# Kernel optimization log

Measured on AMD Instinct MI355X. Metric: run time of the kernel, lower is better.

## Reference

```python
import jax, jax.numpy as jnp
import numpy as np

B, H, S, DK = 2, 16, 2048, 64

def setup_inputs() -> dict:
    key = jax.random.key(0)
    kq, kk, kv, km = jax.random.split(key, 4)
    queries = jax.random.normal(kq, (B, H, S, DK), dtype=jnp.float32)
    keys = jax.random.normal(kk, (B, H, S, DK), dtype=jnp.float32)
    values = jax.random.normal(kv, (B, H, S, DK), dtype=jnp.float32)
    mask = jax.random.randint(km, (B, S, S), 0, 2, dtype=jnp.int32)
    return {"queries": queries, "keys": keys, "values": values, "mask": mask}

def reference(queries, keys, values, mask):
    d_k = queries.shape[-1]
    scale = 1.0 / np.sqrt(d_k).astype(np.float32)
    # [B,H,S,S]
    scores = jnp.einsum('bhqd,bhkd->bhqk', queries, keys) * scale
    m = mask[:, None, :, :]  # broadcast over heads, like mask.unsqueeze(1)
    scores = jnp.where(m == 0, jnp.asarray(-1e9, scores.dtype), scores)
    attn = jax.nn.softmax(scores, axis=-1)
    return jnp.einsum('bhqk,bhkd->bhqd', attn, values)
```

## Files before the change

### kernel.cpp

```cpp
#include <hip/hip_runtime.h>


#define S_   2048
#define D_   64
#define H_   16
#define B_   2
#define BH_  32
#define KVB  64
#define NKV  (S_/KVB)
#define QPB  128
#define NQT  (S_/QPB)

#define KSCALE 0.18033688f

typedef __attribute__((ext_vector_type(8)))  _Float16 f16x8;
typedef __attribute__((ext_vector_type(4)))  _Float16 f16x4;
typedef __attribute__((ext_vector_type(2)))  _Float16 f16x2;
typedef __attribute__((ext_vector_type(4)))  float    f32x4;
typedef __attribute__((ext_vector_type(16))) float    f32x16;
typedef __attribute__((ext_vector_type(4)))  unsigned u32x4;

static __device__ __forceinline__ void async16(const void* g, void* l) {
  __builtin_amdgcn_global_load_lds(
      (const __attribute__((address_space(1))) void*)g,
      (__attribute__((address_space(3))) void*)l, 16, 0, 0);
}

static __device__ __forceinline__ f16x2 pkrtz(float a, float b) {
  return __builtin_bit_cast(f16x2, __builtin_amdgcn_cvt_pkrtz(a, b));
}

static __device__ __forceinline__ void plswap(unsigned& a, unsigned& b, int h) {
#if __has_builtin(__builtin_amdgcn_permlane32_swap)
  auto r = __builtin_amdgcn_permlane32_swap(a, b, false, false);
  a = (unsigned)r[0];
  b = (unsigned)r[1];
#else
  unsigned sa = __shfl_xor(a, 32), sb = __shfl_xor(b, 32);
  unsigned na = h ? sb : a, nb = h ? b : sa;
  a = na; b = nb;
#endif
}

__global__ __launch_bounds__(256) void prepass_k(
    const float* __restrict__ K, const float* __restrict__ V,
    const int* __restrict__ M,
    _Float16* __restrict__ Kh, _Float16* __restrict__ Vth,
    unsigned long long* __restrict__ Mb) {
  __shared__ float tile[64][65];
  const int bidx = blockIdx.x;
  const int tid = threadIdx.x;
  if (bidx < 1024) {
    int st = bidx & 31;
    int bh = bidx >> 5;
    const float* src = V + ((size_t)bh * S_ + st * 64) * D_;
    int r = tid >> 2, cq = tid & 3;
#pragma unroll
    for (int j = 0; j < 4; ++j) {
      float4 v = ((const float4*)(src + (size_t)r * D_))[cq + 4 * j];
      int col = (cq + 4 * j) * 4;
      tile[r][col + 0] = v.x; tile[r][col + 1] = v.y;
      tile[r][col + 2] = v.z; tile[r][col + 3] = v.w;
    }
    __syncthreads();
    int d = tid >> 2, s = (tid & 3) * 16;
    _Float16 tmp[16];
#pragma unroll
    for (int j = 0; j < 16; ++j) tmp[j] = (_Float16)tile[s + j][d];
    _Float16* dstp = Vth + ((size_t)bh * D_ + d) * S_ + st * 64 + s;
    *(f16x8*)(dstp)     = *((f16x8*)tmp);
    *(f16x8*)(dstp + 8) = *((f16x8*)tmp + 1);
  } else if (bidx < 1536) {
    int idx = (bidx - 1024) * 256 + tid;
#pragma unroll
    for (int j = 0; j < 8; ++j) {
      int i = idx + j * 131072;
      float4 v = ((const float4*)K)[i];
      f16x4 o = {(_Float16)(v.x * KSCALE), (_Float16)(v.y * KSCALE),
                 (_Float16)(v.z * KSCALE), (_Float16)(v.w * KSCALE)};
      *(f16x4*)(Kh + 4 * (size_t)i) = o;
    }
  } else {
    int lane = tid & 63;
    int wb = (bidx - 1536) * 256 + (tid >> 6) * 64;
    for (int i = 0; i < 64; ++i) {
      int w = wb + i;
      int m = M[(size_t)w * 64 + lane];
      unsigned long long bal = __ballot(m != 0);
      if (lane == 0) Mb[w] = bal;
    }
  }
}

__global__ __launch_bounds__(256, 2) void attn_fwd(
    const float* __restrict__ Qf, const _Float16* __restrict__ Kh,
    const _Float16* __restrict__ Vth, const unsigned long long* __restrict__ Mb,
    float* __restrict__ Out) {
  __shared__ _Float16 Ks[3][KVB * D_];
  __shared__ _Float16 Vs[3][D_ * KVB];
  __shared__ unsigned long long MLUT[16];

  const int tid = threadIdx.x;
  const int lane = tid & 63;
  const int h = lane >> 5;
  const int c5 = lane & 31;
  const int c7 = c5 & 7;

  if (tid < 16) {
    unsigned w0 = ((tid & 1) ? 0x3C00u : 0u) | ((tid & 2) ? 0x3C000000u : 0u);
    unsigned w1 = ((tid & 4) ? 0x3C00u : 0u) | ((tid & 8) ? 0x3C000000u : 0u);
    MLUT[tid] = (unsigned long long)w0 | ((unsigned long long)w1 << 32);
  }

  int bid = blockIdx.x;
  bid = (bid & 7) * 64 + (bid >> 3);
  const int qt = bid & (NQT - 1);
  const int bh = bid >> 4;
  const int b = bh >> 4;

  const int q = qt * QPB + (tid >> 6) * 32 + c5;

  f16x8 qf[4];
  {
    const float* qp = Qf + ((size_t)bh * S_ + q) * D_ + 8 * h;
#pragma unroll
    for (int dc = 0; dc < 4; ++dc) {
      _Float16 t[8];
#pragma unroll
      for (int j = 0; j < 8; ++j) t[j] = (_Float16)qp[16 * dc + j];
      qf[dc] = *(f16x8*)t;
    }
  }

  f32x16 accO0, accO1;
#pragma unroll
  for (int e = 0; e < 16; ++e) { accO0[e] = 0.f; accO1[e] = 0.f; }
  float l_run = 0.f;

  const int srow = tid >> 3, sgr = tid & 7;
  const int gs = (sgr ^ (srow & 7)) << 3;
  const _Float16* kp = Kh + (size_t)bh * S_ * D_ + (size_t)srow * D_ + gs;
  const _Float16* vp = Vth + (size_t)bh * D_ * S_ + (size_t)srow * S_ + gs;
  const int ldso = (tid & ~63) * 8;
  const unsigned long long* pmb = Mb + ((size_t)b * S_ + q) * NKV;
  const f16x2 one2 = {(_Float16)1.0f, (_Float16)1.0f};

  _Float16 *Kc = &Ks[0][0], *Kn = &Ks[1][0], *Kf = &Ks[2][0];
  _Float16 *Vc = &Vs[0][0], *Vn = &Vs[1][0], *Vf = &Vs[2][0];

#define STAGE(KB, VB, t)                                                    \
  {                                                                         \
    async16(kp + (size_t)(t) * (KVB * D_),            (KB) + ldso);         \
    async16(kp + (size_t)(t) * (KVB * D_) + 32 * D_,  (KB) + ldso + 2048);  \
    async16(vp + (size_t)(t) * KVB,                   (VB) + ldso);         \
    async16(vp + (size_t)(t) * KVB + (size_t)32 * S_, (VB) + ldso + 2048);  \
  }

#define QKT(S0, S1, KB)                                                     \
  {                                                                         \
    _Pragma("unroll") for (int e = 0; e < 16; ++e) { S0[e] = 0.f; S1[e] = 0.f; } \
    __builtin_amdgcn_s_setprio(1);                                          \
    _Pragma("unroll") for (int dc = 0; dc < 4; ++dc) {                      \
      int slot = (((2 * dc + h) ^ c7) << 3);                                \
      f16x8 k0 = *(const f16x8*)(&(KB)[(c5)*D_ + slot]);                    \
      f16x8 k1 = *(const f16x8*)(&(KB)[(32 + c5) * D_ + slot]);             \
      S0 = __builtin_amdgcn_mfma_f32_32x32x16_f16(k0, qf[dc], S0, 0, 0, 0); \
      S1 = __builtin_amdgcn_mfma_f32_32x32x16_f16(k1, qf[dc], S1, 0, 0, 0); \
    }                                                                       \
    __builtin_amdgcn_s_setprio(0);                                          \
  }

#define SOFTMAX_PV(S0, S1, VB, MW)                                          \
  {                                                                         \
    float rs0 = 0.f, rs1 = 0.f;                                             \
    unsigned pkd[2][4][2];                                                  \
    _Pragma("unroll") for (int kt = 0; kt < 2; ++kt) {                      \
      _Pragma("unroll") for (int rr = 0; rr < 4; ++rr) {                    \
        int n = 8 * kt + 2 * rr + h;                                        \
        unsigned nib = (unsigned)((MW) >> (4 * n)) & 0xFu;                  \
        unsigned long long lut = MLUT[nib];                                 \
        f16x2 m01 = __builtin_bit_cast(f16x2, (unsigned)lut);               \
        f16x2 m23 = __builtin_bit_cast(f16x2, (unsigned)(lut >> 32));       \
        float e0 = (kt ? S1[4 * rr + 0] : S0[4 * rr + 0]);                  \
        float e1 = (kt ? S1[4 * rr + 1] : S0[4 * rr + 1]);                  \
        float e2 = (kt ? S1[4 * rr + 2] : S0[4 * rr + 2]);                  \
        float e3 = (kt ? S1[4 * rr + 3] : S0[4 * rr + 3]);                  \
        f16x2 p0 = pkrtz(__builtin_amdgcn_exp2f(e0),                        \
                         __builtin_amdgcn_exp2f(e1)) * m01;                 \
        f16x2 p1 = pkrtz(__builtin_amdgcn_exp2f(e2),                        \
                         __builtin_amdgcn_exp2f(e3)) * m23;                 \
        rs0 = __builtin_amdgcn_fdot2(p0, one2, rs0, false);                 \
        rs1 = __builtin_amdgcn_fdot2(p1, one2, rs1, false);                 \
        pkd[kt][rr][0] = __builtin_bit_cast(unsigned, p0);                  \
        pkd[kt][rr][1] = __builtin_bit_cast(unsigned, p1);                  \
      }                                                                     \
    }                                                                       \
    float rs = rs0 + rs1;                                                   \
    rs += __shfl_xor(rs, 32);                                               \
    l_run += rs;                                                            \
    f16x8 pfrag[4];                                                         \
    _Pragma("unroll") for (int kc = 0; kc < 4; ++kc) {                      \
      int jl = 2 * kc, jh = 2 * kc + 1;                                     \
      unsigned a0 = pkd[jl >> 2][jl & 3][0], a1 = pkd[jl >> 2][jl & 3][1];  \
      unsigned b0 = pkd[jh >> 2][jh & 3][0], b1 = pkd[jh >> 2][jh & 3][1];  \
      plswap(a0, b0, h);                                                    \
      plswap(a1, b1, h);                                                    \
      u32x4 fr = {a0, a1, b0, b1};                                          \
      pfrag[kc] = __builtin_bit_cast(f16x8, fr);                            \
    }                                                                       \
    __builtin_amdgcn_s_setprio(1);                                          \
    _Pragma("unroll") for (int kc = 0; kc < 4; ++kc) {                      \
      int slot = (((2 * kc + h) ^ c7) << 3);                                \
      f16x8 v0 = *(const f16x8*)(&(VB)[(c5)*KVB + slot]);                   \
      f16x8 v1 = *(const f16x8*)(&(VB)[(32 + c5) * KVB + slot]);            \
      accO0 = __builtin_amdgcn_mfma_f32_32x32x16_f16(v0, pfrag[kc], accO0, 0, 0, 0); \
      accO1 = __builtin_amdgcn_mfma_f32_32x32x16_f16(v1, pfrag[kc], accO1, 0, 0, 0); \
    }                                                                       \
    __builtin_amdgcn_s_setprio(0);                                          \
  }

#define ROTATE()                                                            \
  { _Float16* t1 = Kc; Kc = Kn; Kn = Kf; Kf = t1;                           \
    _Float16* t2 = Vc; Vc = Vn; Vn = Vf; Vf = t2; }

#define BODY(R, SC0, SC1, SN0, SN1)                                         \
  {                                                                         \
    __syncthreads();                    \
    unsigned long long mw = mw_next;                                        \
    if ((R) + 1 < NKV) mw_next = pmb[(R) + 1];                              \
    if ((R) + 2 < NKV) STAGE(Kf, Vf, (R) + 2);                              \
    if ((R) + 1 < NKV) QKT(SN0, SN1, Kn);          \
    __builtin_amdgcn_sched_barrier(0);       \
    SOFTMAX_PV(SC0, SC1, Vc, mw);               \
    ROTATE();                                                               \
  }

  f32x16 stA0, stA1, stB0, stB1;

  unsigned long long mw_next = pmb[0];
  STAGE(Kc, Vc, 0);
  STAGE(Kn, Vn, 1);
  __syncthreads();
  QKT(stA0, stA1, Kc);
  __builtin_amdgcn_sched_barrier(0);

  for (int k2 = 0; k2 < NKV / 2; ++k2) {
    BODY(2 * k2,     stA0, stA1, stB0, stB1);
    BODY(2 * k2 + 1, stB0, stB1, stA0, stA1);
  }

  float inv = 1.0f / l_run;
  float* op = Out + ((size_t)bh * S_ + q) * D_;
#pragma unroll
  for (int rr = 0; rr < 4; ++rr) {
    f32x4 o0, o1;
#pragma unroll
    for (int e = 0; e < 4; ++e) {
      o0[e] = accO0[4 * rr + e] * inv;
      o1[e] = accO1[4 * rr + e] * inv;
    }
    *(f32x4*)(op + 8 * rr + 4 * h)      = o0;
    *(f32x4*)(op + 32 + 8 * rr + 4 * h) = o1;
  }
}

extern "C" void kernel_launch(void* const* d_in, const int* in_sizes, int n_in,
                              void* d_out, int out_size, void* d_ws, size_t ws_size,
                              hipStream_t stream) {
  const float* Q = (const float*)d_in[0];
  const float* K = (const float*)d_in[1];
  const float* V = (const float*)d_in[2];
  const int*   M = (const int*)d_in[3];
  float* Out = (float*)d_out;

  const size_t NE = (size_t)B_ * H_ * S_ * D_;
  _Float16* Kh  = (_Float16*)d_ws;
  _Float16* Vth = Kh + NE;
  unsigned long long* Mb = (unsigned long long*)(Vth + NE);

  prepass_k<<<2048, 256, 0, stream>>>(K, V, M, Kh, Vth, Mb);
  attn_fwd<<<NQT * BH_, 256, 0, stream>>>(Q, Kh, Vth, Mb, Out);
}
```

Before: 183.3 us.

## Deepen KV prefetch to four LDS stages with partial vmcnt waits

Grows the K/V shared-memory ring from three to four buffers and prefetches three tiles ahead instead of two. The full __syncthreads is replaced by an explicit partial s_waitcnt vmcnt(5) plus s_barrier, so later async loads can stay in flight. Buffer rotation becomes compile-time indices through a 4x unrolled loop, and the tail is handled by clamped redundant loads rather than branches. This costs more LDS per block, which may reduce occupancy under launch_bounds(256,2), and the vmcnt accounting must match the mask load and the four async loads per stage.

```diff
diff --git a/kernel.cpp b/kernel.cpp
--- a/kernel.cpp
+++ b/kernel.cpp
@@ -96,8 +96,8 @@
     const float* __restrict__ Qf, const _Float16* __restrict__ Kh,
     const _Float16* __restrict__ Vth, const unsigned long long* __restrict__ Mb,
     float* __restrict__ Out) {
-  __shared__ _Float16 Ks[3][KVB * D_];
-  __shared__ _Float16 Vs[3][D_ * KVB];
+  __shared__ _Float16 Ks[4][KVB * D_];
+  __shared__ _Float16 Vs[4][D_ * KVB];
   __shared__ unsigned long long MLUT[16];
 
   const int tid = threadIdx.x;
@@ -145,15 +145,12 @@
   const unsigned long long* pmb = Mb + ((size_t)b * S_ + q) * NKV;
   const f16x2 one2 = {(_Float16)1.0f, (_Float16)1.0f};
 
-  _Float16 *Kc = &Ks[0][0], *Kn = &Ks[1][0], *Kf = &Ks[2][0];
-  _Float16 *Vc = &Vs[0][0], *Vn = &Vs[1][0], *Vf = &Vs[2][0];
-
-#define STAGE(KB, VB, t)                                                    \
-  {                                                                         \
-    async16(kp + (size_t)(t) * (KVB * D_),            (KB) + ldso);         \
-    async16(kp + (size_t)(t) * (KVB * D_) + 32 * D_,  (KB) + ldso + 2048);  \
-    async16(vp + (size_t)(t) * KVB,                   (VB) + ldso);         \
-    async16(vp + (size_t)(t) * KVB + (size_t)32 * S_, (VB) + ldso + 2048);  \
+#define STAGE(SET, t)                                                       \
+  {                                                                         \
+    async16(kp + (size_t)(t) * (KVB * D_),            &Ks[SET][ldso]);      \
+    async16(kp + (size_t)(t) * (KVB * D_) + 32 * D_,  &Ks[SET][ldso + 2048]); \
+    async16(vp + (size_t)(t) * KVB,                   &Vs[SET][ldso]);      \
+    async16(vp + (size_t)(t) * KVB + (size_t)32 * S_, &Vs[SET][ldso + 2048]); \
   }
 
 #define QKT(S0, S1, KB)                                                     \
@@ -219,34 +216,38 @@
     __builtin_amdgcn_s_setprio(0);                                          \
   }
 
-#define ROTATE()                                                            \
-  { _Float16* t1 = Kc; Kc = Kn; Kn = Kf; Kf = t1;                           \
-    _Float16* t2 = Vc; Vc = Vn; Vn = Vf; Vf = t2; }
-
-#define BODY(R, SC0, SC1, SN0, SN1)                                         \
-  {                                                                         \
-    __syncthreads();                    \
+#define BODY(R, SV, SK, SF, SC0, SC1, SN0, SN1)                             \
+  {                                                                         \
+    asm volatile("s_waitcnt vmcnt(5)" ::: "memory");                        \
+    __builtin_amdgcn_sched_barrier(0);                                      \
+    __builtin_amdgcn_s_barrier();                                           \
+    __builtin_amdgcn_sched_barrier(0);                                      \
     unsigned long long mw = mw_next;                                        \
-    if ((R) + 1 < NKV) mw_next = pmb[(R) + 1];                              \
-    if ((R) + 2 < NKV) STAGE(Kf, Vf, (R) + 2);                              \
-    if ((R) + 1 < NKV) QKT(SN0, SN1, Kn);          \
-    __builtin_amdgcn_sched_barrier(0);       \
-    SOFTMAX_PV(SC0, SC1, Vc, mw);               \
-    ROTATE();                                                               \
+    mw_next = pmb[((R) + 1 < NKV) ? (R) + 1 : NKV - 1];                     \
+    STAGE(SF, ((R) + 3 < NKV) ? (R) + 3 : NKV - 1);                         \
+    if ((R) + 1 < NKV) QKT(SN0, SN1, Ks[SK]);                               \
+    __builtin_amdgcn_sched_barrier(0);                                      \
+    SOFTMAX_PV(SC0, SC1, Vs[SV], mw);                                       \
   }
 
   f32x16 stA0, stA1, stB0, stB1;
 
+  STAGE(0, 0);
+  STAGE(1, 1);
   unsigned long long mw_next = pmb[0];
-  STAGE(Kc, Vc, 0);
-  STAGE(Kn, Vn, 1);
-  __syncthreads();
-  QKT(stA0, stA1, Kc);
+  STAGE(2, 2);
+  asm volatile("s_waitcnt vmcnt(5)" ::: "memory");
   __builtin_amdgcn_sched_barrier(0);
-
-  for (int k2 = 0; k2 < NKV / 2; ++k2) {
-    BODY(2 * k2,     stA0, stA1, stB0, stB1);
-    BODY(2 * k2 + 1, stB0, stB1, stA0, stA1);
+  __builtin_amdgcn_s_barrier();
+  QKT(stA0, stA1, Ks[0]);
+  __builtin_amdgcn_sched_barrier(0);
+
+  for (int k4 = 0; k4 < NKV / 4; ++k4) {
+    const int R0 = 4 * k4;
+    BODY(R0 + 0, 0, 1, 3, stA0, stA1, stB0, stB1);
+    BODY(R0 + 1, 1, 2, 0, stB0, stB1, stA0, stA1);
+    BODY(R0 + 2, 2, 3, 1, stA0, stA1, stB0, stB1);
+    BODY(R0 + 3, 3, 0, 2, stB0, stB1, stA0, stA1);
   }
 
   float inv = 1.0f / l_run;
```

Measured after the change: 186.1 us. Within noise of the previous version (+1.5%).
